# Optimization experiments

Hardware: AMD Instinct MI355X
Metric: run time of the kernel (lower is better)

## Reference

```python
import jax, jax.numpy as jnp
from jax import lax
import numpy as np

B, S, G = 64, 200, 8
CHAR_V, GAZ_V = 8000, 100000
D_CHAR, D_GAZ, H = 128, 128, 512
N_LABEL = 20
N_TAG = N_LABEL + 2  # CRF adds START (N_TAG-2) and STOP (N_TAG-1)


def setup_inputs() -> dict:
    key = jax.random.key(0)
    ks = jax.random.split(key, 16)
    lengths = jax.random.randint(ks[0], (B,), S // 2, S + 1)
    pos = jnp.arange(S)[None, :]
    mask = pos < lengths[:, None]
    char_inputs = jax.random.randint(ks[1], (B, S), 0, CHAR_V)
    gaz_ids = jax.random.randint(ks[2], (B, S, G), 0, GAZ_V)
    cnt = jax.random.randint(ks[3], (B, S), 1, G + 1)
    gaz_mask = (jnp.arange(G)[None, None, :] < cnt[..., None]).astype(jnp.int32)
    rev_gaz_ids = jax.random.randint(ks[4], (B, S, G), 0, GAZ_V)
    rcnt = jax.random.randint(ks[5], (B, S), 1, G + 1)
    rev_gaz_mask = (jnp.arange(G)[None, None, :] < rcnt[..., None]).astype(jnp.int32)
    sc = 0.1
    D_in = D_CHAR + D_GAZ
    return dict(
        char_inputs=char_inputs, lengths=lengths, mask=mask,
        gaz_ids=gaz_ids, gaz_mask=gaz_mask,
        rev_gaz_ids=rev_gaz_ids, rev_gaz_mask=rev_gaz_mask,
        char_table=jax.random.normal(ks[6], (CHAR_V, D_CHAR)) * sc,
        gaz_table=jax.random.normal(ks[7], (GAZ_V, D_GAZ)) * sc,
        w_ih_f=jax.random.normal(ks[8], (4 * H, D_in)) * sc,
        w_hh_f=jax.random.normal(ks[9], (4 * H, H)) * sc,
        b_f=jnp.zeros((4 * H,), jnp.float32),
        w_ih_b=jax.random.normal(ks[10], (4 * H, D_in)) * sc,
        w_hh_b=jax.random.normal(ks[11], (4 * H, H)) * sc,
        b_b=jnp.zeros((4 * H,), jnp.float32),
        W_out=jax.random.normal(ks[12], (2 * H, N_TAG)) * sc,
        b_out=jnp.zeros((N_TAG,), jnp.float32),
        transitions=jax.random.normal(ks[13], (N_TAG, N_TAG)) * sc,
    )


def rev_pad(x, lengths):
    # reverse each sequence within its valid length (reverse_padded_sequence)
    b, s = x.shape[0], x.shape[1]
    pos = jnp.arange(s)[None, :]
    idx = jnp.where(pos < lengths[:, None], lengths[:, None] - 1 - pos, pos)
    idx = idx.reshape((b, s) + (1,) * (x.ndim - 2))
    return jnp.take_along_axis(x, jnp.broadcast_to(idx, x.shape), axis=1)


def gaz_embed(table, ids, m):
    # masked mean over the G candidate gaz words per char (Gaz_Embed, type=1)
    e = table[ids]                                   # [B,S,G,D]
    mf = m.astype(e.dtype)[..., None]
    return (e * mf).sum(2) / jnp.maximum(mf.sum(2), 1.0)


def lstm(x, w_ih, w_hh, b):
    # x: [B,S,D]; torch gate order i,f,g,o
    h0 = jnp.zeros((x.shape[0], H), x.dtype)

    def step(carry, xt):
        h, c = carry
        g = xt @ w_ih.T + h @ w_hh.T + b
        i, f, gg, o = jnp.split(g, 4, axis=-1)
        c = jax.nn.sigmoid(f) * c + jax.nn.sigmoid(i) * jnp.tanh(gg)
        h = jax.nn.sigmoid(o) * jnp.tanh(c)
        return (h, c), h

    _, hs = lax.scan(step, (h0, h0), x.transpose(1, 0, 2))
    return hs.transpose(1, 0, 2)                     # [B,S,H]


def emissions_fn(char_inputs, lengths, gaz_ids, gaz_mask, rev_gaz_ids, rev_gaz_mask,
                 char_table, gaz_table, w_ih_f, w_hh_f, b_f, w_ih_b, w_hh_b, b_b,
                 W_out, b_out):
    char_embs = char_table[char_inputs]              # [B,S,Dc]
    rev_char_embs = rev_pad(char_embs, lengths)
    g_f = gaz_embed(gaz_table, gaz_ids, gaz_mask)
    g_b = gaz_embed(gaz_table, rev_pad(rev_gaz_ids, lengths), rev_pad(rev_gaz_mask, lengths))
    fwd_in = jnp.concatenate([char_embs, g_f], axis=-1)
    bwd_in = jnp.concatenate([rev_char_embs, g_b], axis=-1)
    h_f = lstm(fwd_in, w_ih_f, w_hh_f, b_f)
    h_b = rev_pad(lstm(bwd_in, w_ih_b, w_hh_b, b_b), lengths)
    lstm_outs = jnp.concatenate([h_f, h_b], axis=-1)  # [B,S,2H]
    return lstm_outs @ W_out + b_out                  # [B,S,N_TAG]


def viterbi(emissions, mask, transitions):
    # transitions[prev, next]; START=N_TAG-2, STOP=N_TAG-1
    n = emissions.shape[-1]
    start, stop = n - 2, n - 1
    init = emissions[:, 0] + transitions[start][None, :]     # [B,n]
    ident = jnp.arange(n, dtype=jnp.int32)[None, :]

    def vstep(part, inp):
        emit_t, m_t = inp                                    # [B,n], [B]
        cand = part[:, :, None] + transitions[None] + emit_t[:, None, :]
        new = cand.max(axis=1)
        bp = cand.argmax(axis=1).astype(jnp.int32)
        part = jnp.where(m_t[:, None], new, part)
        bp = jnp.where(m_t[:, None], bp, ident)              # identity bp on pad
        return part, bp

    part, bps = lax.scan(vstep, init,
                         (emissions[:, 1:].transpose(1, 0, 2), mask[:, 1:].T))
    last_tag = (part + transitions[:, stop][None, :]).argmax(-1).astype(jnp.int32)

    def btstep(tag, bp):
        prev = jnp.take_along_axis(bp, tag[:, None], axis=1)[:, 0]
        return prev, prev

    _, prev_tags = lax.scan(btstep, last_tag, bps, reverse=True)  # [S-1,B]
    tags = jnp.concatenate([prev_tags.T, last_tag[:, None]], axis=1)
    return tags * mask.astype(tags.dtype)


def reference(char_inputs, lengths, mask, gaz_ids, gaz_mask, rev_gaz_ids, rev_gaz_mask,
              char_table, gaz_table, w_ih_f, w_hh_f, b_f, w_ih_b, w_hh_b, b_b,
              W_out, b_out, transitions):
    emissions = emissions_fn(char_inputs, lengths, gaz_ids, gaz_mask,
                             rev_gaz_ids, rev_gaz_mask, char_table, gaz_table,
                             w_ih_f, w_hh_f, b_f, w_ih_b, w_hh_b, b_b, W_out, b_out)
    return viterbi(emissions, mask, transitions)
```

## Files before the change

### kernel.cpp

```cpp
#include <hip/hip_runtime.h>
#include <math.h>

#define S_LEN 200
#define BATCH 64
#define HID   512
#define NTAG  22
#define TCH   40
#define MC    (TCH*BATCH)
#define HSTR  (HID*BATCH + 256)
#define ASTR  64

typedef unsigned short u16;
typedef unsigned int   u32;

__device__ __forceinline__ float bf2f(u16 u){
  union { u32 ui; float f; } v; v.ui = ((u32)u) << 16; return v.f;
}

__device__ __forceinline__ float rdlane(float x, int lane){
  return __int_as_float(__builtin_amdgcn_readlane(__float_as_int(x), lane));
}

__global__ void k_detect(const u32* __restrict__ w, int* __restrict__ flag){
  __shared__ int cnt;
  if (threadIdx.x == 0) cnt = 0;
  __syncthreads();
  int hits = 0;
  for (int i = threadIdx.x; i < 16384; i += 256){
    u32 e = (w[i] & 0x7F80u);
    if (e >= 0x3800u && e <= 0x4080u) hits++;
  }
  atomicAdd(&cnt, hits);
  __syncthreads();
  if (threadIdx.x == 0) *flag = (cnt > 8192) ? 1 : 0;
}

__global__ void k_cvt_f(const void* __restrict__ src, float* __restrict__ dst,
                        int n, const int* __restrict__ flag){
  int i = blockIdx.x*blockDim.x + threadIdx.x;
  if (i >= n) return;
  if (*flag) dst[i] = bf2f(((const u16*)src)[i]);
  else       dst[i] = ((const float*)src)[i];
}

__global__ void k_cvt_wt(const void* __restrict__ src, float* __restrict__ dst,
                         const int* __restrict__ flag){
  int i = blockIdx.x*blockDim.x + threadIdx.x;
  if (i >= 1024*24) return;
  int k = i / 24, tag = i % 24;
  float v = 0.f;
  if (tag < NTAG){
    v = (*flag) ? bf2f(((const u16*)src)[k*NTAG + tag])
                : ((const float*)src)[k*NTAG + tag];
  }
  int half = k >> 9, kk = k & 511;
  dst[((size_t)half*512 + kk)*24 + tag] = v;
}

__global__ void k_zero(float* __restrict__ p, int n){
  int i = blockIdx.x*blockDim.x + threadIdx.x;
  if (i < n) p[i] = 0.f;
}

__global__ __launch_bounds__(128)
void k_build(const int* __restrict__ ci, const int* __restrict__ lengths,
             const int* __restrict__ gid, const int* __restrict__ gm,
             const int* __restrict__ rgid, const int* __restrict__ rgm,
             const void* __restrict__ ctab, const void* __restrict__ gtab,
             const int* __restrict__ flag,
             float* __restrict__ fin, float* __restrict__ bin)
{
  int bs = blockIdx.x;
  int b = bs / S_LEN, s = bs % S_LEN;
  int d = threadIdx.x;
  int isbf = *flag;
  int len = lengths[b];
  int sb = (s < len) ? (len - 1 - s) : s;
  size_t orow = ((size_t)s*BATCH + b)*256;

  {
    int cid = ci[bs];
    float cv = isbf ? bf2f(((const u16*)ctab)[(size_t)cid*128 + d])
                    : ((const float*)ctab)[(size_t)cid*128 + d];
    fin[orow + d] = cv;
    const int* gg = gid + (size_t)bs*8;
    const int* mm = gm  + (size_t)bs*8;
    float sum = 0.f, cntf = 0.f;
    for (int g = 0; g < 8; ++g){
      float m = (float)mm[g];
      int gw = gg[g];
      float gv = isbf ? bf2f(((const u16*)gtab)[(size_t)gw*128 + d])
                      : ((const float*)gtab)[(size_t)gw*128 + d];
      sum += m * gv; cntf += m;
    }
    fin[orow + 128 + d] = sum / fmaxf(cntf, 1.f);
  }
  {
    int bsr = b*S_LEN + sb;
    int cid = ci[bsr];
    float cv = isbf ? bf2f(((const u16*)ctab)[(size_t)cid*128 + d])
                    : ((const float*)ctab)[(size_t)cid*128 + d];
    bin[orow + d] = cv;
    const int* gg = rgid + (size_t)bsr*8;
    const int* mm = rgm  + (size_t)bsr*8;
    float sum = 0.f, cntf = 0.f;
    for (int g = 0; g < 8; ++g){
      float m = (float)mm[g];
      int gw = gg[g];
      float gv = isbf ? bf2f(((const u16*)gtab)[(size_t)gw*128 + d])
                      : ((const float*)gtab)[(size_t)gw*128 + d];
      sum += m * gv; cntf += m;
    }
    bin[orow + 128 + d] = sum / fmaxf(cntf, 1.f);
  }
}

__global__ __launch_bounds__(256)
void k_gemm_ih(const float* __restrict__ Af, const float* __restrict__ Ab,
               const float* __restrict__ wih,
               const float* __restrict__ bias,
               float* __restrict__ gxc,
               int t0)
{
  const int dir = blockIdx.z;
  const float* A = (dir ? Ab : Af) + (size_t)t0*BATCH*256;
  const float* W = wih + (size_t)dir*2048*256;
  const float* bi = bias + (size_t)dir*2048;
  float* C = gxc + (size_t)dir*2048*MC;
  const int m0 = blockIdx.y * 128;
  const int n0 = blockIdx.x * 128;
  const int tid = threadIdx.x;

  __shared__ float As[32][132];
  __shared__ float Ws[32][132];

  const int lrow = tid >> 3;
  const int lk   = (tid & 7) * 4;

  const int tx = tid & 15;
  const int ty = tid >> 4;

  float acc[8][8] = {};

  for (int k0 = 0; k0 < 256; k0 += 32){
    #pragma unroll
    for (int q = 0; q < 4; ++q){
      const int row = lrow + q*32;
      float4 a = *(const float4*)(A + (size_t)(m0+row)*256 + k0 + lk);
      float4 w = *(const float4*)(W + (size_t)(n0+row)*256 + k0 + lk);
      As[lk+0][row]=a.x; As[lk+1][row]=a.y; As[lk+2][row]=a.z; As[lk+3][row]=a.w;
      Ws[lk+0][row]=w.x; Ws[lk+1][row]=w.y; Ws[lk+2][row]=w.z; Ws[lk+3][row]=w.w;
    }
    __syncthreads();
    #pragma unroll 8
    for (int kk = 0; kk < 32; ++kk){
      float4 a0 = *(const float4*)(&As[kk][ty*8]);
      float4 a1 = *(const float4*)(&As[kk][ty*8+4]);
      float4 w0 = *(const float4*)(&Ws[kk][tx*8]);
      float4 w1 = *(const float4*)(&Ws[kk][tx*8+4]);
      float am[8] = {a0.x,a0.y,a0.z,a0.w,a1.x,a1.y,a1.z,a1.w};
      float wn[8] = {w0.x,w0.y,w0.z,w0.w,w1.x,w1.y,w1.z,w1.w};
      #pragma unroll
      for (int i = 0; i < 8; ++i)
        #pragma unroll
        for (int jj = 0; jj < 8; ++jj)
          acc[i][jj] += am[i]*wn[jj];
    }
    __syncthreads();
  }

  #pragma unroll
  for (int jj = 0; jj < 8; ++jj){
    const int n = n0 + tx*8 + jj;
    const float bj = bi[n];
    #pragma unroll
    for (int i = 0; i < 8; i += 4){
      float4 o = make_float4(acc[i][jj]+bj, acc[i+1][jj]+bj,
                             acc[i+2][jj]+bj, acc[i+3][jj]+bj);
      *(float4*)(C + (size_t)n*MC + m0 + ty*8 + i) = o;
    }
  }
}

__global__ __launch_bounds__(512, 1)
void k_lstm(const float* __restrict__ whh,
            const float* __restrict__ gxc,
            float* __restrict__ cbuf,
            float* __restrict__ hseq,
            int* __restrict__ arr,
            int t0)
{
  const int dir = blockIdx.x >> 7;
  const int hrow_base = (blockIdx.x & 127) * 4;
  const int tid = threadIdx.x;
  const int b = tid & 63;
  const int uw = __builtin_amdgcn_readfirstlane(tid >> 6);
  const int uk0 = uw * 64;

  __shared__ float wl[4*4*512];
  __shared__ float part[8*16*64];

  const float* whhd = whh + (size_t)dir*2048*512;

  #pragma unroll
  for (int g = 0; g < 4; ++g){
    float4 v = *(const float4*)(whhd + ((size_t)g*512 + hrow_base)*512 + tid*4);
    *(float4*)(&wl[g*2048 + tid*4]) = v;
  }

  const int hr  = tid >> 6;
  const int hrow = hrow_base + (hr & 3);
  float creg = 0.f;
  if (tid < 256)
    creg = cbuf[((size_t)dir*HID + hrow)*BATCH + b];
  __syncthreads();

  for (int tc = 0; tc < TCH; ++tc){
    const int t = t0 + tc;

    float gx0 = 0.f, gx1 = 0.f, gx2 = 0.f, gx3 = 0.f;
    if (tid < 256){
      const float* gxb = gxc + (size_t)dir*2048*MC + (size_t)tc*BATCH + b;
      gx0 = gxb[(size_t)(   0 + hrow)*MC];
      gx1 = gxb[(size_t)( 512 + hrow)*MC];
      gx2 = gxb[(size_t)(1024 + hrow)*MC];
      gx3 = gxb[(size_t)(1536 + hrow)*MC];
    }

    if (t > 0){
      if (tid == 0){
        const int* a = arr + (((size_t)(t-1)*2 + dir)*8)*ASTR;
        int s = 0;
        while (s < 128){
          s = 0;
          #pragma unroll
          for (int q = 0; q < 8; ++q)
            s += __hip_atomic_load(&a[q*ASTR], __ATOMIC_RELAXED,
                                   __HIP_MEMORY_SCOPE_AGENT);
          if (s < 128) __builtin_amdgcn_s_sleep(1);
        }
      }
      __syncthreads();
    }

    float hv[64];
    if (t > 0){
      const float* hbase = hseq + ((size_t)dir*S_LEN + (t-1))*HSTR;
      #pragma unroll
      for (int j = 0; j < 64; ++j)
        hv[j] = hbase[(size_t)(uk0 + j)*BATCH + b];
    } else {
      #pragma unroll
      for (int j = 0; j < 64; ++j) hv[j] = 0.f;
    }

    float acc[16];
    #pragma unroll
    for (int r = 0; r < 16; ++r) acc[r] = 0.f;

    #pragma unroll
    for (int r = 0; r < 16; ++r){
      const float* wr = &wl[(r >> 2)*2048 + (r & 3)*512 + uk0];
      #pragma unroll
      for (int j4 = 0; j4 < 16; ++j4){
        float4 w = *(const float4*)(wr + j4*4);
        acc[r] += w.x*hv[4*j4] + w.y*hv[4*j4+1] + w.z*hv[4*j4+2] + w.w*hv[4*j4+3];
      }
    }

    #pragma unroll
    for (int r = 0; r < 16; ++r)
      part[(uw*16 + r)*64 + b] = acc[r];
    __syncthreads();

    if (tid < 256){
      float g4[4];
      #pragma unroll
      for (int g = 0; g < 4; ++g){
        const int r = g*4 + hr;
        float s = 0.f;
        #pragma unroll
        for (int ww = 0; ww < 8; ++ww)
          s += part[(ww*16 + r)*64 + b];
        g4[g] = s;
      }
      float gi = g4[0] + gx0;
      float gf = g4[1] + gx1;
      float gg = g4[2] + gx2;
      float go = g4[3] + gx3;
      float si = 1.f/(1.f+expf(-gi));
      float sf = 1.f/(1.f+expf(-gf));
      float so = 1.f/(1.f+expf(-go));
      creg = sf*creg + si*tanhf(gg);
      float h = so*tanhf(creg);
      float* hdst = hseq + ((size_t)dir*S_LEN + t)*HSTR + (size_t)hrow*BATCH + b;
      __hip_atomic_store(hdst, h, __ATOMIC_RELAXED, __HIP_MEMORY_SCOPE_AGENT);
    }
    __syncthreads();

    if (tid == 0)
      __hip_atomic_fetch_add(
          arr + (((size_t)t*2 + dir)*8 + (blockIdx.x & 7))*ASTR, 1,
          __ATOMIC_RELAXED, __HIP_MEMORY_SCOPE_AGENT);
  }

  if (tid < 256)
    cbuf[((size_t)dir*HID + hrow)*BATCH + b] = creg;
}

__global__ __launch_bounds__(256)
void k_emis(const float* __restrict__ hseq, const int* __restrict__ lengths,
            const float* __restrict__ wpad,
            const float* __restrict__ bout,
            float* __restrict__ emisF, float* __restrict__ emisB)
{
  const int t = blockIdx.x;
  const int dir = blockIdx.y;
  const int tid = threadIdx.x;
  const int b = tid & 63;
  const int utg = __builtin_amdgcn_readfirstlane(tid >> 6);

  __shared__ float hl[64*64];

  const float* hsrc = hseq + ((size_t)(dir*S_LEN + t))*HSTR;
  const float* wbase = wpad + (size_t)dir*512*24 + utg*6;

  float acc[6] = {0.f,0.f,0.f,0.f,0.f,0.f};

  for (int c = 0; c < 8; ++c){
    const float4* s4 = (const float4*)(hsrc + (size_t)c*64*64);
    float4* d4 = (float4*)hl;
    #pragma unroll
    for (int q = 0; q < 4; ++q) d4[q*256 + tid] = s4[q*256 + tid];
    __syncthreads();
    const float* wrow = wbase + (size_t)c*64*24;
    #pragma unroll 4
    for (int k = 0; k < 64; ++k){
      float hval = hl[k*64 + b];
      #pragma unroll
      for (int i = 0; i < 6; ++i) acc[i] += hval * wrow[k*24 + i];
    }
    __syncthreads();
  }

  const int len = lengths[b];
  const int pos = dir ? ((t < len) ? (len - 1 - t) : t) : t;
  float* dst = (dir ? emisB : emisF) + ((size_t)b*S_LEN + pos)*NTAG;
  #pragma unroll
  for (int i = 0; i < 6; ++i){
    int tag = utg*6 + i;
    if (tag < NTAG) dst[tag] = acc[i] + (dir ? 0.f : bout[tag]);
  }
}

__global__ __launch_bounds__(64)
void k_viterbi(const float* __restrict__ emisF, const float* __restrict__ emisB,
               const int* __restrict__ lengths,
               const float* __restrict__ trans, int* __restrict__ out)
{
  const int b = blockIdx.x;
  const int j = threadIdx.x;
  __shared__ float esum[S_LEN*NTAG];
  __shared__ unsigned char bp[(S_LEN-1)*NTAG];

  const float* ef = emisF + (size_t)b*S_LEN*NTAG;
  const float* eb = emisB + (size_t)b*S_LEN*NTAG;
  for (int i = j; i < S_LEN*NTAG; i += 64) esum[i] = ef[i] + eb[i];

  const int len = lengths[b];
  float trr[NTAG];
  #pragma unroll
  for (int i = 0; i < NTAG; ++i)
    trr[i] = (j < NTAG) ? trans[i*NTAG + j] : 0.f;
  __syncthreads();

  float p = (j < NTAG) ? (esum[j] + trans[(NTAG-2)*NTAG + j]) : -3.4e38f;

  for (int t = 1; t < S_LEN; ++t){
    float v[NTAG];
    #pragma unroll
    for (int i = 0; i < NTAG; ++i)
      v[i] = rdlane(p, i) + trr[i];
    float m1[11]; int x1[11];
    #pragma unroll
    for (int i = 0; i < 11; ++i){
      const bool g = v[2*i+1] > v[2*i];
      m1[i] = g ? v[2*i+1] : v[2*i];
      x1[i] = g ? 2*i+1 : 2*i;
    }
    float m2[6]; int x2[6];
    #pragma unroll
    for (int i = 0; i < 5; ++i){
      const bool g = m1[2*i+1] > m1[2*i];
      m2[i] = g ? m1[2*i+1] : m1[2*i];
      x2[i] = g ? x1[2*i+1] : x1[2*i];
    }
    m2[5] = m1[10]; x2[5] = x1[10];
    float m3[3]; int x3[3];
    #pragma unroll
    for (int i = 0; i < 3; ++i){
      const bool g = m2[2*i+1] > m2[2*i];
      m3[i] = g ? m2[2*i+1] : m2[2*i];
      x3[i] = g ? x2[2*i+1] : x2[2*i];
    }
    const bool g01 = m3[1] > m3[0];
    float mm = g01 ? m3[1] : m3[0];
    int   xx = g01 ? x3[1] : x3[0];
    const bool g2 = m3[2] > mm;
    mm = g2 ? m3[2] : mm;
    xx = g2 ? x3[2] : xx;

    const float e = esum[t*NTAG + j];
    if (j < NTAG)
      bp[(t-1)*NTAG + j] = (unsigned char)((t < len) ? xx : j);
    p = (t < len) ? (mm + e) : p;
  }
  __syncthreads();

  if (j == 0){
    float best = -3.4e38f; int tag = 0;
    #pragma unroll
    for (int i = 0; i < NTAG; ++i){
      float vv = rdlane(p, i) + trans[i*NTAG + (NTAG-1)];
      if (vv > best){ best = vv; tag = i; }
    }
    out[b*S_LEN + S_LEN-1] = (S_LEN-1 < len) ? tag : 0;
    for (int t = S_LEN-2; t >= 0; --t){
      tag = bp[t*NTAG + tag];
      out[b*S_LEN + t] = (t < len) ? tag : 0;
    }
  }
}

extern "C" void kernel_launch(void* const* d_in, const int* in_sizes, int n_in,
                              void* d_out, int out_size, void* d_ws, size_t ws_size,
                              hipStream_t stream)
{
  (void)in_sizes; (void)n_in; (void)out_size; (void)ws_size;
  const int* char_inputs  = (const int*)d_in[0];
  const int* lengths      = (const int*)d_in[1];
  const int* gaz_ids      = (const int*)d_in[3];
  const int* gaz_mask     = (const int*)d_in[4];
  const int* rev_gaz_ids  = (const int*)d_in[5];
  const int* rev_gaz_mask = (const int*)d_in[6];
  const void* char_table  = d_in[7];
  const void* gaz_table   = d_in[8];
  const void* w_ih_f = d_in[9];
  const void* w_hh_f = d_in[10];
  const void* b_f    = d_in[11];
  const void* w_ih_b = d_in[12];
  const void* w_hh_b = d_in[13];
  const void* b_b    = d_in[14];
  const void* W_out  = d_in[15];
  const void* b_out  = d_in[16];
  const void* trans  = d_in[17];

  char* ws = (char*)d_ws;
  size_t off = 0;
  auto alloc = [&](size_t bytes)->char*{
    char* p = ws + off; off = (off + bytes + 255) & ~(size_t)255; return p;
  };
  int*   flag   = (int*)  alloc(256);
  float* whh32  = (float*)alloc(2ull*2048*512*4);
  float* wih32  = (float*)alloc(2ull*2048*256*4);
  float* bias32 = (float*)alloc(2ull*2048*4);
  float* wpad   = (float*)alloc(2ull*512*24*4);
  float* bout32 = (float*)alloc(22ull*4);
  float* trans32= (float*)alloc(484ull*4);
  float* fwd_in = (float*)alloc(12800ull*256*4);
  float* bwd_in = (float*)alloc(12800ull*256*4);
  float* gxc    = (float*)alloc(2ull*2048*MC*4);
  float* cbuf   = (float*)alloc(2ull*512*64*4);
  int*   arrival= (int*)  alloc(200ull*2*8*ASTR*4);
  float* hseq   = (float*)alloc(2ull*200*HSTR*4);
  float* emisF  = (float*)alloc(12800ull*22*4);
  float* emisB  = (float*)alloc(12800ull*22*4);

  k_detect<<<1,256,0,stream>>>((const u32*)char_table, flag);
  k_cvt_f<<<4096,256,0,stream>>>(w_hh_f, whh32,           1048576, flag);
  k_cvt_f<<<4096,256,0,stream>>>(w_hh_b, whh32 + 1048576, 1048576, flag);
  k_cvt_f<<<2048,256,0,stream>>>(w_ih_f, wih32,            524288, flag);
  k_cvt_f<<<2048,256,0,stream>>>(w_ih_b, wih32 + 524288,   524288, flag);
  k_cvt_f<<<8,256,0,stream>>>(b_f, bias32,        2048, flag);
  k_cvt_f<<<8,256,0,stream>>>(b_b, bias32 + 2048, 2048, flag);
  k_cvt_wt<<<96,256,0,stream>>>(W_out, wpad, flag);
  k_cvt_f<<<1,256,0,stream>>>(b_out, bout32, 22, flag);
  k_cvt_f<<<2,256,0,stream>>>(trans, trans32, 484, flag);

  k_build<<<12800,128,0,stream>>>(char_inputs, lengths, gaz_ids, gaz_mask,
                                  rev_gaz_ids, rev_gaz_mask, char_table, gaz_table,
                                  flag, fwd_in, bwd_in);

  k_zero<<<256,256,0,stream>>>(cbuf, 2*512*64);
  k_zero<<<800,256,0,stream>>>((float*)arrival, 200*2*8*ASTR);

  for (int t0 = 0; t0 < S_LEN; t0 += TCH){
    k_gemm_ih<<<dim3(16,MC/128,2),256,0,stream>>>(fwd_in, bwd_in, wih32, bias32,
                                                  gxc, t0);
    hipLaunchKernelGGL(k_lstm, dim3(256), dim3(512), 0, stream,
                       whh32, gxc, cbuf, hseq, arrival, t0);
  }

  k_emis<<<dim3(S_LEN,2),256,0,stream>>>(hseq, lengths, wpad, bout32, emisF, emisB);
  k_viterbi<<<64,64,0,stream>>>(emisF, emisB, lengths, trans32, (int*)d_out);
}
```

Baseline: 2.563 ms.

## Replace block-wide counter wait with per-wave waits on the producing block group

```diff
diff --git a/kernel.cpp b/kernel.cpp
--- a/kernel.cpp
+++ b/kernel.cpp
@@ -191,7 +191,8 @@
             int t0)
 {
   const int dir = blockIdx.x >> 7;
-  const int hrow_base = (blockIdx.x & 127) * 4;
+  const int lb  = blockIdx.x & 127;
+  const int hrow_base = lb * 4;
   const int tid = threadIdx.x;
   const int b = tid & 63;
   const int uw = __builtin_amdgcn_readfirstlane(tid >> 6);
@@ -227,25 +228,22 @@
       gx3 = gxb[(size_t)(1536 + hrow)*MC];
     }
 
+    int hoff = 0;
     if (t > 0){
-      if (tid == 0){
-        const int* a = arr + (((size_t)(t-1)*2 + dir)*8)*ASTR;
-        int s = 0;
-        while (s < 128){
-          s = 0;
-          #pragma unroll
-          for (int q = 0; q < 8; ++q)
-            s += __hip_atomic_load(&a[q*ASTR], __ATOMIC_RELAXED,
-                                   __HIP_MEMORY_SCOPE_AGENT);
-          if (s < 128) __builtin_amdgcn_s_sleep(1);
-        }
-      }
-      __syncthreads();
+      const int* a = arr + (((size_t)(t-1)*2 + dir)*8 + uw)*ASTR;
+      int c;
+      do {
+        c = __hip_atomic_load(a, __ATOMIC_RELAXED, __HIP_MEMORY_SCOPE_AGENT);
+        if (c < 16) __builtin_amdgcn_s_sleep(1);
+      } while (c < 16);
+      c = __hip_atomic_load(a, __ATOMIC_ACQUIRE, __HIP_MEMORY_SCOPE_AGENT);
+      hoff = c >> 5;
+      asm volatile("" : "+v"(hoff) : : "memory");
     }
 
     float hv[64];
     if (t > 0){
-      const float* hbase = hseq + ((size_t)dir*S_LEN + (t-1))*HSTR;
+      const float* hbase = hseq + ((size_t)dir*S_LEN + (t-1))*HSTR + hoff;
       #pragma unroll
       for (int j = 0; j < 64; ++j)
         hv[j] = hbase[(size_t)(uk0 + j)*BATCH + b];
@@ -300,8 +298,8 @@
 
     if (tid == 0)
       __hip_atomic_fetch_add(
-          arr + (((size_t)t*2 + dir)*8 + (blockIdx.x & 7))*ASTR, 1,
-          __ATOMIC_RELAXED, __HIP_MEMORY_SCOPE_AGENT);
+          arr + (((size_t)t*2 + dir)*8 + (lb >> 4))*ASTR, 1,
+          __ATOMIC_RELEASE, __HIP_MEMORY_SCOPE_AGENT);
   }
 
   if (tid < 256)
```

Result: slower. 6.127 ms (+139.1%).
